# Kernel optimization log

Measured on AMD Instinct MI355X. Metric: run time of the kernel, lower is better.

Reference implementation:

```python
import jax, jax.numpy as jnp
import numpy as np

C = 256   # in_channels
H = 48
W = 48
B = 2     # batch after chunking into 3 frames; input batch = 3*B
F = 3     # frames (torch.chunk(x, 3))
G = 4     # GroupNorm groups
EPS = 1e-6


def setup_inputs() -> dict:
    key = jax.random.key(0)
    ks = jax.random.split(key, 10)
    s = C ** -0.5  # keep q/k magnitudes sane so softmax is not saturated
    return {
        "x":    jax.random.normal(ks[0], (F * B, C, H, W), jnp.float32),
        "gn_w": jnp.ones((C,), jnp.float32),
        "gn_b": jnp.zeros((C,), jnp.float32),
        "wq":   jax.random.normal(ks[1], (C, C), jnp.float32) * s,
        "bq":   jax.random.normal(ks[2], (C,), jnp.float32) * 0.02,
        "wk":   jax.random.normal(ks[3], (C, C), jnp.float32) * s,
        "bk":   jax.random.normal(ks[4], (C,), jnp.float32) * 0.02,
        "wv":   jax.random.normal(ks[5], (C, C), jnp.float32) * s,
        "bv":   jax.random.normal(ks[6], (C,), jnp.float32) * 0.02,
        "wp":   jax.random.normal(ks[7], (C, C), jnp.float32) * s,
        "bp":   jax.random.normal(ks[8], (C,), jnp.float32) * 0.02,
    }


def reference(x, gn_w, gn_b, wq, bq, wk, bk, wv, bv, wp, bp):
    B3, c, h, w = x.shape
    b = B3 // F
    # torch.chunk(x, 3) + stack(dim=2) -> (b, c, f, h, w); chunk index is frame
    hx = jnp.moveaxis(x.reshape(F, b, c, h, w), 0, 2)  # (b, c, f, h, w)

    # GroupNorm(num_groups=4, eps=1e-6, affine)
    hg = hx.reshape(b, G, c // G, F, h, w)
    mu = hg.mean(axis=(2, 3, 4, 5), keepdims=True)
    var = hg.var(axis=(2, 3, 4, 5), keepdims=True)
    hn = ((hg - mu) * jax.lax.rsqrt(var + EPS)).reshape(b, c, F, h, w)
    hn = hn * gn_w[None, :, None, None, None] + gn_b[None, :, None, None, None]

    # 1x1x1 Conv3d == channel matmul over flattened tokens n = (f h w)
    n = F * h * w
    hf = hn.reshape(b, c, n)                                  # (b, c, n)
    q = jnp.einsum('oc,bcn->bon', wq, hf) + bq[None, :, None]
    k = jnp.einsum('oc,bcn->bon', wk, hf) + bk[None, :, None]
    v = jnp.einsum('oc,bcn->bon', wv, hf) + bv[None, :, None]

    # scores[b,n,m] = sum_c q[b,c,n] * k[b,c,m], scaled by c^-0.5, softmax over m
    scores = jnp.einsum('bcn,bcm->bnm', q, k) * (c ** -0.5)
    attn = jax.nn.softmax(scores, axis=-1)                    # (b, n, n)

    # out[b,c,n] = sum_m v[b,c,m] * attn[b,n,m]
    o = jnp.einsum('bcm,bnm->bcn', v, attn)
    o = jnp.einsum('oc,bcn->bon', wp, o) + bp[None, :, None]  # proj_out

    o = o.reshape(b, c, F, h, w)
    # permute(0,2,1,3,4) then merge (b f) -> batch (b-major, f-minor)
    o = jnp.moveaxis(o, 2, 1).reshape(B3, c, h, w)
    return x + o
```

## Files before the change

### kernel.cpp

```cpp
#include <hip/hip_runtime.h>
#include <stdint.h>

#define CDIM 256
#define HW 2304
#define FR 3
#define NBATCH 2
#define NTOK 6912
#define EPSV 1e-6f
#define QSCALE (0.0625f * 1.44269504088896f)

typedef __attribute__((ext_vector_type(8))) short short8;
typedef __attribute__((ext_vector_type(4))) short short4v;
typedef __attribute__((ext_vector_type(4))) float f32x4;
typedef unsigned short u16;

__device__ inline u16 f2bf(float f) {
  union { float f; uint32_t u; } v; v.f = f;
  uint32_t r = v.u + 0x7FFFu + ((v.u >> 16) & 1u);
  return (u16)(r >> 16);
}
__device__ inline float bf2f(u16 h) {
  union { uint32_t u; float f; } v; v.u = ((uint32_t)h) << 16; return v.f;
}
__device__ inline void gload16(const void* g, void* l) {
  __builtin_amdgcn_global_load_lds(
      (const __attribute__((address_space(1))) void*)g,
      (__attribute__((address_space(3))) void*)l, 16, 0, 0);
}

__global__ void pre_k(const float* x, float* part, const float* wq,
                      const float* wk, const float* wv, const float* wp,
                      u16* wb) {
  if (blockIdx.x >= 256) {
    int idx = (blockIdx.x - 256) * 256 + threadIdx.x;
    wb[0 * 65536 + idx] = f2bf(wq[idx] * QSCALE);
    wb[1 * 65536 + idx] = f2bf(wk[idx]);
    wb[2 * 65536 + idx] = f2bf(wv[idx]);
    wb[3 * 65536 + idx] = f2bf(wp[idx]);
    return;
  }
  int bg = blockIdx.x >> 5, sl = blockIdx.x & 31;
  int b = bg >> 2, g = bg & 3;
  int tid = threadIdx.x;
  float s1 = 0.f, s2 = 0.f;
  for (int i = tid; i < 2 * NTOK; i += 256) {
    int cl = sl * 2 + (i / NTOK); int rem = i % NTOK;
    int f = rem / HW; int hw = rem - f * HW;
    float v = x[((size_t)(f * NBATCH + b) * CDIM + g * 64 + cl) * HW + hw];
    s1 += v; s2 += v * v;
  }
  #pragma unroll
  for (int m = 32; m >= 1; m >>= 1) {
    s1 += __shfl_xor(s1, m, 64);
    s2 += __shfl_xor(s2, m, 64);
  }
  __shared__ float r1[4], r2[4];
  int wid = tid >> 6;
  if ((tid & 63) == 0) { r1[wid] = s1; r2[wid] = s2; }
  __syncthreads();
  if (tid == 0) {
    part[blockIdx.x * 2 + 0] = r1[0] + r1[1] + r1[2] + r1[3];
    part[blockIdx.x * 2 + 1] = r2[0] + r2[1] + r2[2] + r2[3];
  }
}

__global__ void gn_fin_k(const float* part, float* stats) {
  int tid = threadIdx.x;
  if (tid < 8) {
    float s1 = 0.f, s2 = 0.f;
    for (int s = 0; s < 32; ++s) {
      s1 += part[(tid * 32 + s) * 2 + 0];
      s2 += part[(tid * 32 + s) * 2 + 1];
    }
    float inv = 1.f / (64.f * NTOK);
    float mu = s1 * inv;
    float var = s2 * inv - mu * mu;
    stats[tid * 2 + 0] = mu;
    stats[tid * 2 + 1] = rsqrtf(var + EPSV);
  }
}

__global__ void gn_apply_k(const float* x, const float* gn_w, const float* gn_b,
                           const float* stats, u16* hn) {
  int nt = blockIdx.x, ct = blockIdx.y, b = blockIdx.z;
  int tid = threadIdx.x;
  __shared__ float tile[64][65];
  int n0 = nt * 64; int f = n0 / HW; int hw0 = n0 - f * HW;
  float mu = stats[(b * 4 + ct) * 2 + 0];
  float rs = stats[(b * 4 + ct) * 2 + 1];
  #pragma unroll
  for (int i = 0; i < 16; ++i) {
    int lin = i * 256 + tid;
    int cr = lin >> 6, nc = lin & 63;
    int c = ct * 64 + cr;
    float v = x[((size_t)(f * NBATCH + b) * CDIM + c) * HW + hw0 + nc];
    tile[cr][nc] = (v - mu) * rs * gn_w[c] + gn_b[c];
  }
  __syncthreads();
  #pragma unroll
  for (int i = 0; i < 16; ++i) {
    int lin = i * 256 + tid;
    int nr = lin >> 6, cc = lin & 63;
    hn[((size_t)b * NTOK + n0 + nr) * CDIM + ct * 64 + cc] = f2bf(tile[cc][nr]);
  }
}

__global__ __launch_bounds__(256) void qkv_k(const u16* hn, const u16* wb,
    const float* bq, const float* bk, const float* bv,
    u16* qb, u16* kb, u16* vb) {
  int nt = blockIdx.x;
  int op = blockIdx.y >> 1, b = blockIdx.y & 1;
  int tid = threadIdx.x, lane = tid & 63, wid = tid >> 6;
  int lr = lane & 15, lg = lane >> 4;
  __shared__ __align__(16) char hn_lds[32768];
  {
    const char* src = (const char*)(hn + ((size_t)b * NTOK + nt * 64) * CDIM);
    #pragma unroll
    for (int i = 0; i < 8; ++i) {
      int off = i * 4096 + wid * 1024 + lane * 16;
      int row = off >> 9;
      gload16(src + (off ^ ((row & 7) << 4)), hn_lds + i * 4096 + wid * 1024);
    }
  }
  __syncthreads();
  f32x4 acc[16];
  #pragma unroll
  for (int i = 0; i < 16; ++i) acc[i] = (f32x4){0.f, 0.f, 0.f, 0.f};
  const u16* wsrc = wb + op * 65536;
  __builtin_amdgcn_s_setprio(1);
  #pragma unroll
  for (int cc = 0; cc < 4; ++cc) {
    short8 afr[2];
    #pragma unroll
    for (int kc = 0; kc < 2; ++kc) {
      int row = wid * 16 + lr;
      int byte = row * 512 + (cc * 64 + kc * 32 + lg * 8) * 2;
      afr[kc] = *(const short8*)(hn_lds + (byte ^ ((row & 7) << 4)));
    }
    #pragma unroll
    for (int cot = 0; cot < 16; ++cot) {
      #pragma unroll
      for (int kc = 0; kc < 2; ++kc) {
        short8 bfr = *(const short8*)(wsrc + (size_t)(cot * 16 + lr) * CDIM +
                                      cc * 64 + kc * 32 + lg * 8);
        if (op == 2)
          acc[cot] = __builtin_amdgcn_mfma_f32_16x16x32_bf16(afr[kc], bfr, acc[cot], 0, 0, 0);
        else
          acc[cot] = __builtin_amdgcn_mfma_f32_16x16x32_bf16(bfr, afr[kc], acc[cot], 0, 0, 0);
      }
    }
  }
  __builtin_amdgcn_s_setprio(0);
  if (op == 2) {
    int m0 = wid * 16 + lg * 4;
    char* vtile = (char*)vb + (size_t)b * NTOK * CDIM * 2 + (size_t)nt * 32768;
    int mchunk = (m0 >> 3);
    #pragma unroll
    for (int cot = 0; cot < 16; ++cot) {
      int co = cot * 16 + lr;
      float bb = bv[co];
      short4v r;
      #pragma unroll
      for (int j = 0; j < 4; ++j) r[j] = (short)f2bf(acc[cot][j] + bb);
      *(short4v*)(vtile + mchunk * 4096 + co * 16 + (lg & 1) * 8) = r;
    }
  } else {
    int row = wid * 16 + lr;
    int n = nt * 64 + row;
    const float* bias = (op == 0) ? bq : bk;
    float bscale = (op == 0) ? QSCALE : 1.0f;
    char* ktile = (char*)kb + (size_t)b * NTOK * CDIM * 2 + (size_t)nt * 32768;
    #pragma unroll
    for (int cot = 0; cot < 16; ++cot) {
      int co = cot * 16 + lg * 4;
      f32x4 b4 = *(const f32x4*)(bias + co);
      short4v r;
      #pragma unroll
      for (int j = 0; j < 4; ++j) r[j] = (short)f2bf(acc[cot][j] + b4[j] * bscale);
      if (op == 0) {
        *(short4v*)(qb + ((size_t)b * NTOK + n) * CDIM + co) = r;
      } else {
        int colchunk = cot * 2 + (lg >> 1);
        *(short4v*)(ktile + colchunk * 1024 + row * 16 + (lg & 1) * 8) = r;
      }
    }
  }
}

template <bool SPLIT>
__global__ __launch_bounds__(768, 3) void flash_k(const u16* qb, const u16* kb,
                                                  const u16* vb, u16* opart,
                                                  float* ml, u16* ob) {
  int qt = blockIdx.x, b = blockIdx.y, sp = blockIdx.z;
  int tid = threadIdx.x, lane = tid & 63, wid = tid >> 6;
  int lr = lane & 15, lg = lane >> 4;
  __shared__ __align__(16) char k_lds[2][32768];
  __shared__ __align__(16) char v_lds[2][32768];
  __shared__ __align__(16) char p_lds[12][2048];

  int t0 = SPLIT ? 36 * sp : 0;
  int t1 = SPLIT ? 36 * sp + 36 : 108;

  short8 aq[8];
  int nq = qt * 192 + wid * 16 + lr;
  const u16* qsrc = qb + ((size_t)b * NTOK + nq) * CDIM;
  #pragma unroll
  for (int kc = 0; kc < 8; ++kc) aq[kc] = *(const short8*)(qsrc + kc * 32 + lg * 8);

  float mrun = -1e30f, lrun = 0.f;
  f32x4 acc[16];
  #pragma unroll
  for (int i = 0; i < 16; ++i) acc[i] = (f32x4){0.f, 0.f, 0.f, 0.f};

  const char* kbb = (const char*)(kb + (size_t)b * NTOK * CDIM);
  const char* vbb = (const char*)(vb + (size_t)b * NTOK * CDIM);
  char* pw = p_lds[wid];
  int kqoff = lg * 1024 + lr * 16;
  int pvoff = lg * 4096 + lr * 16;

  {
    const char* ks = kbb + (size_t)t0 * 32768;
    const char* vs = vbb + (size_t)t0 * 32768;
    for (int ch = wid; ch < 64; ch += 12) {
      if (ch < 32) gload16(ks + ch * 1024 + lane * 16, k_lds[0] + ch * 1024);
      else gload16(vs + (ch - 32) * 1024 + lane * 16, v_lds[0] + (ch - 32) * 1024);
    }
  }
  __syncthreads();

  for (int t = t0; t < t1; ++t) {
    int cur = (t - t0) & 1;
    if (t + 1 < t1) {
      const char* ks = kbb + (size_t)(t + 1) * 32768;
      const char* vs = vbb + (size_t)(t + 1) * 32768;
      for (int ch = wid; ch < 64; ch += 12) {
        if (ch < 32) gload16(ks + ch * 1024 + lane * 16, k_lds[cur ^ 1] + ch * 1024);
        else gload16(vs + (ch - 32) * 1024 + lane * 16, v_lds[cur ^ 1] + (ch - 32) * 1024);
      }
    }
    const char* kcur = k_lds[cur] + kqoff;
    const char* vcur = v_lds[cur] + pvoff;
    f32x4 s[4];
    __builtin_amdgcn_s_setprio(1);
    #pragma unroll
    for (int mt = 0; mt < 4; ++mt) {
      f32x4 a = (f32x4){0.f, 0.f, 0.f, 0.f};
      #pragma unroll
      for (int kc = 0; kc < 8; ++kc) {
        short8 kf = *(const short8*)(kcur + kc * 4096 + mt * 256);
        a = __builtin_amdgcn_mfma_f32_16x16x32_bf16(kf, aq[kc], a, 0, 0, 0);
      }
      s[mt] = a;
    }
    __builtin_amdgcn_s_setprio(0);
    float m0 = fmaxf(fmaxf(s[0][0], s[0][1]), fmaxf(s[0][2], s[0][3]));
    float m1 = fmaxf(fmaxf(s[1][0], s[1][1]), fmaxf(s[1][2], s[1][3]));
    float m2 = fmaxf(fmaxf(s[2][0], s[2][1]), fmaxf(s[2][2], s[2][3]));
    float m3 = fmaxf(fmaxf(s[3][0], s[3][1]), fmaxf(s[3][2], s[3][3]));
    float pmax = fmaxf(fmaxf(m0, m1), fmaxf(m2, m3));
    pmax = fmaxf(pmax, __shfl_xor(pmax, 16, 64));
    pmax = fmaxf(pmax, __shfl_xor(pmax, 32, 64));
    if (__any(pmax > mrun + 6.0f)) {
      float mn = fmaxf(mrun, pmax);
      float r = exp2f(mrun - mn);
      mrun = mn; lrun *= r;
      #pragma unroll
      for (int i = 0; i < 16; ++i) {
        acc[i][0] *= r; acc[i][1] *= r; acc[i][2] *= r; acc[i][3] *= r;
      }
    }
    float ls = 0.f;
    #pragma unroll
    for (int mt = 0; mt < 4; ++mt) {
      #pragma unroll
      for (int j = 0; j < 4; ++j) {
        float p = exp2f(s[mt][j] - mrun);
        s[mt][j] = p;
        ls += p;
      }
    }
    ls += __shfl_xor(ls, 16, 64);
    ls += __shfl_xor(ls, 32, 64);
    lrun += ls;
    #pragma unroll
    for (int mt = 0; mt < 4; ++mt) {
      #pragma unroll
      for (int tp = 0; tp < 2; ++tp) {
        uint32_t pk;
        asm("v_cvt_pk_bf16_f32 %0, %1, %2"
            : "=v"(pk) : "v"(s[mt][2 * tp]), "v"(s[mt][2 * tp + 1]));
        int byte = lr * 128 + mt * 32 + lg * 8 + tp * 4;
        *(uint32_t*)(pw + (byte ^ ((lr & 7) << 4))) = pk;
      }
    }
    __builtin_amdgcn_s_setprio(1);
    #pragma unroll
    for (int mc = 0; mc < 2; ++mc) {
      int pb = lr * 128 + mc * 64 + lg * 16;
      short8 bfr = *(const short8*)(pw + (pb ^ ((lr & 7) << 4)));
      #pragma unroll
      for (int ct = 0; ct < 16; ++ct) {
        short8 av = *(const short8*)(vcur + mc * 16384 + ct * 256);
        acc[ct] = __builtin_amdgcn_mfma_f32_16x16x32_bf16(av, bfr, acc[ct], 0, 0, 0);
      }
    }
    __builtin_amdgcn_s_setprio(0);
    __syncthreads();
  }

  if (!SPLIT) {
    float linv = 1.0f / lrun;
    u16* d0 = ob + ((size_t)b * NTOK + nq) * CDIM;
    #pragma unroll
    for (int ct = 0; ct < 16; ++ct) {
      short4v r;
      #pragma unroll
      for (int j = 0; j < 4; ++j) r[j] = (short)f2bf(acc[ct][j] * linv);
      *(short4v*)(d0 + ct * 16 + lg * 4) = r;
    }
  } else {
    u16* d0 = opart + ((size_t)(sp * 2 + b) * NTOK + nq) * CDIM;
    #pragma unroll
    for (int ct = 0; ct < 16; ++ct) {
      short4v r;
      #pragma unroll
      for (int j = 0; j < 4; ++j) r[j] = (short)f2bf(acc[ct][j]);
      *(short4v*)(d0 + ct * 16 + lg * 4) = r;
    }
    if (lg == 0) {
      size_t mb = (size_t)(sp * 2 + b) * 2;
      ml[(mb + 0) * NTOK + nq] = mrun;
      ml[(mb + 1) * NTOK + nq] = lrun;
    }
  }
}

template <bool SPLIT>
__global__ __launch_bounds__(256) void proj_k(const u16* ob, const u16* opart,
    const float* ml, const u16* wb, const float* bp, const float* x, float* out) {
  int nt = blockIdx.x, b = blockIdx.y;
  int tid = threadIdx.x, lane = tid & 63, wid = tid >> 6;
  int lr = lane & 15, lg = lane >> 4;
  __shared__ __align__(16) char o_lds[32768];
  const u16* wpb = wb + 3 * 65536;
  if (SPLIT) {
    #pragma unroll
    for (int i = 0; i < 8; ++i) {
      int off = i * 4096 + tid * 16;
      int row = off >> 9;
      int c0 = (off & 511) >> 1;
      int n = nt * 64 + row;
      float mm[3], llv[3];
      #pragma unroll
      for (int s = 0; s < 3; ++s) {
        mm[s] = ml[((size_t)(s * 2 + b) * 2 + 0) * NTOK + n];
        llv[s] = ml[((size_t)(s * 2 + b) * 2 + 1) * NTOK + n];
      }
      float M = fmaxf(fmaxf(mm[0], mm[1]), mm[2]);
      float w[3]; float den = 0.f;
      #pragma unroll
      for (int s = 0; s < 3; ++s) { w[s] = exp2f(mm[s] - M); den += w[s] * llv[s]; }
      float inv = 1.f / den;
      float o[8] = {0.f, 0.f, 0.f, 0.f, 0.f, 0.f, 0.f, 0.f};
      #pragma unroll
      for (int s = 0; s < 3; ++s) {
        short8 v = *(const short8*)(opart + ((size_t)(s * 2 + b) * NTOK + n) * CDIM + c0);
        #pragma unroll
        for (int j = 0; j < 8; ++j) o[j] += w[s] * bf2f((u16)v[j]);
      }
      short8 r8;
      #pragma unroll
      for (int j = 0; j < 8; ++j) r8[j] = (short)f2bf(o[j] * inv);
      *(short8*)(o_lds + (off ^ ((row & 7) << 4))) = r8;
    }
  } else {
    const char* src = (const char*)(ob + ((size_t)b * NTOK + nt * 64) * CDIM);
    #pragma unroll
    for (int i = 0; i < 8; ++i) {
      int off = i * 4096 + wid * 1024 + lane * 16;
      int row = off >> 9;
      gload16(src + (off ^ ((row & 7) << 4)), o_lds + i * 4096 + wid * 1024);
    }
  }
  __syncthreads();
  #pragma unroll
  for (int ct2 = 0; ct2 < 4; ++ct2) {
    int cot = wid * 4 + ct2;
    short8 aw[8];
    #pragma unroll
    for (int kc = 0; kc < 8; ++kc)
      aw[kc] = *(const short8*)(wpb + (size_t)(cot * 16 + lr) * CDIM + kc * 32 + lg * 8);
    #pragma unroll
    for (int ntile = 0; ntile < 4; ++ntile) {
      f32x4 a = (f32x4){0.f, 0.f, 0.f, 0.f};
      #pragma unroll
      for (int kc = 0; kc < 8; ++kc) {
        int row = ntile * 16 + lr;
        int byte = row * 512 + (kc * 32 + lg * 8) * 2;
        short8 bfr = *(const short8*)(o_lds + (byte ^ ((row & 7) << 4)));
        a = __builtin_amdgcn_mfma_f32_16x16x32_bf16(aw[kc], bfr, a, 0, 0, 0);
      }
      int n = nt * 64 + ntile * 16 + lr;
      int f = n / HW; int hw = n - f * HW;
      #pragma unroll
      for (int j = 0; j < 4; ++j) {
        int co = cot * 16 + lg * 4 + j;
        float val = a[j] + bp[co];
        size_t oi = ((size_t)(b * FR + f) * CDIM + co) * HW + hw;
        out[oi] = x[oi] + val;
      }
    }
  }
}

extern "C" void kernel_launch(void* const* d_in, const int* in_sizes, int n_in,
                              void* d_out, int out_size, void* d_ws, size_t ws_size,
                              hipStream_t stream) {
  const float* x    = (const float*)d_in[0];
  const float* gn_w = (const float*)d_in[1];
  const float* gn_b = (const float*)d_in[2];
  const float* wq   = (const float*)d_in[3];
  const float* bq   = (const float*)d_in[4];
  const float* wk   = (const float*)d_in[5];
  const float* bk   = (const float*)d_in[6];
  const float* wv   = (const float*)d_in[7];
  const float* bv   = (const float*)d_in[8];
  const float* wp   = (const float*)d_in[9];
  const float* bp   = (const float*)d_in[10];
  float* out = (float*)d_out;
  char* ws = (char*)d_ws;

  float* stats = (float*)(ws + 0);
  float* part  = (float*)(ws + 256);
  u16* wb = (u16*)(ws + 4096);
  u16* hn = (u16*)(ws + 528384);
  u16* qb = (u16*)(ws + 7606272);
  u16* kb = (u16*)(ws + 14684160);
  u16* vb = (u16*)(ws + 21762048);
  u16* ob = (u16*)(ws + 28839936);
  u16* opart = (u16*)(ws + 35917824);
  float* ml  = (float*)(ws + 57151488);
  const size_t NEED_SPLIT = 57483264;

  pre_k<<<512, 256, 0, stream>>>(x, part, wq, wk, wv, wp, wb);
  gn_fin_k<<<1, 64, 0, stream>>>(part, stats);
  gn_apply_k<<<dim3(108, 4, 2), 256, 0, stream>>>(x, gn_w, gn_b, stats, hn);
  qkv_k<<<dim3(108, 6), 256, 0, stream>>>(hn, wb, bq, bk, bv, qb, kb, vb);
  if (ws_size >= NEED_SPLIT) {
    flash_k<true><<<dim3(36, 2, 3), 768, 0, stream>>>(qb, kb, vb, opart, ml, ob);
    proj_k<true><<<dim3(108, 2), 256, 0, stream>>>(ob, opart, ml, wb, bp, x, out);
  } else {
    flash_k<false><<<dim3(36, 2, 1), 768, 0, stream>>>(qb, kb, vb, opart, ml, ob);
    proj_k<false><<<dim3(108, 2), 256, 0, stream>>>(ob, opart, ml, wb, bp, x, out);
  }
}
```

Before: 227.2 us.

## Rewrite flash attention with 32x32x16 MFMA and in-register P via permlane swap

Result: faster. 216.3 us, median of 2 (-4.8%).

```diff
diff --git a/kernel.cpp b/kernel.cpp
--- a/kernel.cpp
+++ b/kernel.cpp
@@ -12,6 +12,8 @@
 typedef __attribute__((ext_vector_type(8))) short short8;
 typedef __attribute__((ext_vector_type(4))) short short4v;
 typedef __attribute__((ext_vector_type(4))) float f32x4;
+typedef __attribute__((ext_vector_type(16))) float f32x16;
+typedef __attribute__((ext_vector_type(4))) uint32_t u32x4;
 typedef unsigned short u16;
 
 __device__ inline u16 f2bf(float f) {
@@ -188,42 +190,45 @@
 }
 
 template <bool SPLIT>
-__global__ __launch_bounds__(768, 3) void flash_k(const u16* qb, const u16* kb,
+__global__ __launch_bounds__(512, 2) void flash_k(const u16* qb, const u16* kb,
                                                   const u16* vb, u16* opart,
                                                   float* ml, u16* ob) {
   int qt = blockIdx.x, b = blockIdx.y, sp = blockIdx.z;
   int tid = threadIdx.x, lane = tid & 63, wid = tid >> 6;
-  int lr = lane & 15, lg = lane >> 4;
+  int ln = lane & 31, hi = lane >> 5;
   __shared__ __align__(16) char k_lds[2][32768];
   __shared__ __align__(16) char v_lds[2][32768];
-  __shared__ __align__(16) char p_lds[12][2048];
-
-  int t0 = SPLIT ? 36 * sp : 0;
-  int t1 = SPLIT ? 36 * sp + 36 : 108;
-
-  short8 aq[8];
-  int nq = qt * 192 + wid * 16 + lr;
+
+  int t0 = SPLIT ? 27 * sp : 0;
+  int t1 = SPLIT ? 27 * sp + 27 : 108;
+
+  int nq = qt * 256 + wid * 32 + ln;
   const u16* qsrc = qb + ((size_t)b * NTOK + nq) * CDIM;
-  #pragma unroll
-  for (int kc = 0; kc < 8; ++kc) aq[kc] = *(const short8*)(qsrc + kc * 32 + lg * 8);
+  short8 qf[16];
+  #pragma unroll
+  for (int ks = 0; ks < 16; ++ks)
+    qf[ks] = *(const short8*)(qsrc + ks * 16 + hi * 8);
 
   float mrun = -1e30f, lrun = 0.f;
-  f32x4 acc[16];
-  #pragma unroll
-  for (int i = 0; i < 16; ++i) acc[i] = (f32x4){0.f, 0.f, 0.f, 0.f};
+  f32x16 o[8];
+  #pragma unroll
+  for (int i = 0; i < 8; ++i)
+    #pragma unroll
+    for (int j = 0; j < 16; ++j) o[i][j] = 0.f;
 
   const char* kbb = (const char*)(kb + (size_t)b * NTOK * CDIM);
   const char* vbb = (const char*)(vb + (size_t)b * NTOK * CDIM);
-  char* pw = p_lds[wid];
-  int kqoff = lg * 1024 + lr * 16;
-  int pvoff = lg * 4096 + lr * 16;
+  int kbase = hi * 1024 + ln * 16;
+  int vbase = hi * 4096 + ln * 16;
 
   {
-    const char* ks = kbb + (size_t)t0 * 32768;
-    const char* vs = vbb + (size_t)t0 * 32768;
-    for (int ch = wid; ch < 64; ch += 12) {
-      if (ch < 32) gload16(ks + ch * 1024 + lane * 16, k_lds[0] + ch * 1024);
-      else gload16(vs + (ch - 32) * 1024 + lane * 16, v_lds[0] + (ch - 32) * 1024);
+    const char* ks_ = kbb + (size_t)t0 * 32768;
+    const char* vs_ = vbb + (size_t)t0 * 32768;
+    #pragma unroll
+    for (int i = 0; i < 8; ++i) {
+      int ch = i * 8 + wid;
+      if (ch < 32) gload16(ks_ + ch * 1024 + lane * 16, k_lds[0] + ch * 1024);
+      else gload16(vs_ + (ch - 32) * 1024 + lane * 16, v_lds[0] + (ch - 32) * 1024);
     }
   }
   __syncthreads();
@@ -231,80 +236,72 @@
   for (int t = t0; t < t1; ++t) {
     int cur = (t - t0) & 1;
     if (t + 1 < t1) {
-      const char* ks = kbb + (size_t)(t + 1) * 32768;
-      const char* vs = vbb + (size_t)(t + 1) * 32768;
-      for (int ch = wid; ch < 64; ch += 12) {
-        if (ch < 32) gload16(ks + ch * 1024 + lane * 16, k_lds[cur ^ 1] + ch * 1024);
-        else gload16(vs + (ch - 32) * 1024 + lane * 16, v_lds[cur ^ 1] + (ch - 32) * 1024);
-      }
-    }
-    const char* kcur = k_lds[cur] + kqoff;
-    const char* vcur = v_lds[cur] + pvoff;
-    f32x4 s[4];
-    __builtin_amdgcn_s_setprio(1);
-    #pragma unroll
-    for (int mt = 0; mt < 4; ++mt) {
-      f32x4 a = (f32x4){0.f, 0.f, 0.f, 0.f};
-      #pragma unroll
-      for (int kc = 0; kc < 8; ++kc) {
-        short8 kf = *(const short8*)(kcur + kc * 4096 + mt * 256);
-        a = __builtin_amdgcn_mfma_f32_16x16x32_bf16(kf, aq[kc], a, 0, 0, 0);
-      }
-      s[mt] = a;
-    }
-    __builtin_amdgcn_s_setprio(0);
-    float m0 = fmaxf(fmaxf(s[0][0], s[0][1]), fmaxf(s[0][2], s[0][3]));
-    float m1 = fmaxf(fmaxf(s[1][0], s[1][1]), fmaxf(s[1][2], s[1][3]));
-    float m2 = fmaxf(fmaxf(s[2][0], s[2][1]), fmaxf(s[2][2], s[2][3]));
-    float m3 = fmaxf(fmaxf(s[3][0], s[3][1]), fmaxf(s[3][2], s[3][3]));
-    float pmax = fmaxf(fmaxf(m0, m1), fmaxf(m2, m3));
-    pmax = fmaxf(pmax, __shfl_xor(pmax, 16, 64));
-    pmax = fmaxf(pmax, __shfl_xor(pmax, 32, 64));
-    if (__any(pmax > mrun + 6.0f)) {
-      float mn = fmaxf(mrun, pmax);
-      float r = exp2f(mrun - mn);
-      mrun = mn; lrun *= r;
-      #pragma unroll
-      for (int i = 0; i < 16; ++i) {
-        acc[i][0] *= r; acc[i][1] *= r; acc[i][2] *= r; acc[i][3] *= r;
-      }
-    }
-    float ls = 0.f;
-    #pragma unroll
-    for (int mt = 0; mt < 4; ++mt) {
-      #pragma unroll
-      for (int j = 0; j < 4; ++j) {
-        float p = exp2f(s[mt][j] - mrun);
-        s[mt][j] = p;
-        ls += p;
-      }
-    }
-    ls += __shfl_xor(ls, 16, 64);
-    ls += __shfl_xor(ls, 32, 64);
-    lrun += ls;
-    #pragma unroll
-    for (int mt = 0; mt < 4; ++mt) {
-      #pragma unroll
-      for (int tp = 0; tp < 2; ++tp) {
-        uint32_t pk;
-        asm("v_cvt_pk_bf16_f32 %0, %1, %2"
-            : "=v"(pk) : "v"(s[mt][2 * tp]), "v"(s[mt][2 * tp + 1]));
-        int byte = lr * 128 + mt * 32 + lg * 8 + tp * 4;
-        *(uint32_t*)(pw + (byte ^ ((lr & 7) << 4))) = pk;
-      }
-    }
-    __builtin_amdgcn_s_setprio(1);
-    #pragma unroll
-    for (int mc = 0; mc < 2; ++mc) {
-      int pb = lr * 128 + mc * 64 + lg * 16;
-      short8 bfr = *(const short8*)(pw + (pb ^ ((lr & 7) << 4)));
-      #pragma unroll
-      for (int ct = 0; ct < 16; ++ct) {
-        short8 av = *(const short8*)(vcur + mc * 16384 + ct * 256);
-        acc[ct] = __builtin_amdgcn_mfma_f32_16x16x32_bf16(av, bfr, acc[ct], 0, 0, 0);
-      }
-    }
-    __builtin_amdgcn_s_setprio(0);
+      const char* ks_ = kbb + (size_t)(t + 1) * 32768;
+      const char* vs_ = vbb + (size_t)(t + 1) * 32768;
+      #pragma unroll
+      for (int i = 0; i < 8; ++i) {
+        int ch = i * 8 + wid;
+        if (ch < 32) gload16(ks_ + ch * 1024 + lane * 16, k_lds[cur ^ 1] + ch * 1024);
+        else gload16(vs_ + (ch - 32) * 1024 + lane * 16, v_lds[cur ^ 1] + (ch - 32) * 1024);
+      }
+    }
+    const char* kc = k_lds[cur] + kbase;
+    const char* vc = v_lds[cur] + vbase;
+
+    #pragma unroll
+    for (int mt = 0; mt < 2; ++mt) {
+      f32x16 S;
+      #pragma unroll
+      for (int j = 0; j < 16; ++j) S[j] = 0.f;
+      __builtin_amdgcn_s_setprio(1);
+      #pragma unroll
+      for (int ks = 0; ks < 16; ++ks) {
+        short8 kf = *(const short8*)(kc + ks * 2048 + mt * 512);
+        S = __builtin_amdgcn_mfma_f32_32x32x16_bf16(kf, qf[ks], S, 0, 0, 0);
+      }
+      __builtin_amdgcn_s_setprio(0);
+      float px = S[0];
+      #pragma unroll
+      for (int j = 1; j < 16; ++j) px = fmaxf(px, S[j]);
+      px = fmaxf(px, __shfl_xor(px, 32, 64));
+      if (__any(px > mrun + 10.0f)) {
+        float mn = fmaxf(mrun, px);
+        float r = exp2f(mrun - mn);
+        mrun = mn; lrun *= r;
+        #pragma unroll
+        for (int i = 0; i < 8; ++i)
+          #pragma unroll
+          for (int j = 0; j < 16; ++j) o[i][j] *= r;
+      }
+      float lsum = 0.f;
+      #pragma unroll
+      for (int j = 0; j < 16; ++j) {
+        float p = exp2f(S[j] - mrun);
+        S[j] = p; lsum += p;
+      }
+      lsum += __shfl_xor(lsum, 32, 64);
+      lrun += lsum;
+      #pragma unroll
+      for (int lks = 0; lks < 2; ++lks) {
+        int rb = lks * 8;
+        uint32_t x0, x1, y0, y1;
+        asm("v_cvt_pk_bf16_f32 %0, %1, %2" : "=v"(x0) : "v"(S[rb + 0]), "v"(S[rb + 1]));
+        asm("v_cvt_pk_bf16_f32 %0, %1, %2" : "=v"(x1) : "v"(S[rb + 2]), "v"(S[rb + 3]));
+        asm("v_cvt_pk_bf16_f32 %0, %1, %2" : "=v"(y0) : "v"(S[rb + 4]), "v"(S[rb + 5]));
+        asm("v_cvt_pk_bf16_f32 %0, %1, %2" : "=v"(y1) : "v"(S[rb + 6]), "v"(S[rb + 7]));
+        asm("v_permlane32_swap_b32 %0, %1" : "+v"(x0), "+v"(y0));
+        asm("v_permlane32_swap_b32 %0, %1" : "+v"(x1), "+v"(y1));
+        u32x4 pd = (u32x4){x0, x1, y0, y1};
+        short8 pf = *(short8*)&pd;
+        __builtin_amdgcn_s_setprio(1);
+        #pragma unroll
+        for (int ct = 0; ct < 8; ++ct) {
+          short8 vf = *(const short8*)(vc + (mt * 2 + lks) * 8192 + ct * 512);
+          o[ct] = __builtin_amdgcn_mfma_f32_32x32x16_bf16(vf, pf, o[ct], 0, 0, 0);
+        }
+        __builtin_amdgcn_s_setprio(0);
+      }
+    }
     __syncthreads();
   }
 
@@ -312,22 +309,28 @@
     float linv = 1.0f / lrun;
     u16* d0 = ob + ((size_t)b * NTOK + nq) * CDIM;
     #pragma unroll
-    for (int ct = 0; ct < 16; ++ct) {
-      short4v r;
-      #pragma unroll
-      for (int j = 0; j < 4; ++j) r[j] = (short)f2bf(acc[ct][j] * linv);
-      *(short4v*)(d0 + ct * 16 + lg * 4) = r;
+    for (int ct = 0; ct < 8; ++ct) {
+      #pragma unroll
+      for (int rq = 0; rq < 4; ++rq) {
+        short4v r4;
+        #pragma unroll
+        for (int j = 0; j < 4; ++j) r4[j] = (short)f2bf(o[ct][rq * 4 + j] * linv);
+        *(short4v*)(d0 + ct * 32 + rq * 8 + hi * 4) = r4;
+      }
     }
   } else {
     u16* d0 = opart + ((size_t)(sp * 2 + b) * NTOK + nq) * CDIM;
     #pragma unroll
-    for (int ct = 0; ct < 16; ++ct) {
-      short4v r;
-      #pragma unroll
-      for (int j = 0; j < 4; ++j) r[j] = (short)f2bf(acc[ct][j]);
-      *(short4v*)(d0 + ct * 16 + lg * 4) = r;
-    }
-    if (lg == 0) {
+    for (int ct = 0; ct < 8; ++ct) {
+      #pragma unroll
+      for (int rq = 0; rq < 4; ++rq) {
+        short4v r4;
+        #pragma unroll
+        for (int j = 0; j < 4; ++j) r4[j] = (short)f2bf(o[ct][rq * 4 + j]);
+        *(short4v*)(d0 + ct * 32 + rq * 8 + hi * 4) = r4;
+      }
+    }
+    if (hi == 0) {
       size_t mb = (size_t)(sp * 2 + b) * 2;
       ml[(mb + 0) * NTOK + nq] = mrun;
       ml[(mb + 1) * NTOK + nq] = lrun;
@@ -350,20 +353,20 @@
       int row = off >> 9;
       int c0 = (off & 511) >> 1;
       int n = nt * 64 + row;
-      float mm[3], llv[3];
-      #pragma unroll
-      for (int s = 0; s < 3; ++s) {
+      float mm[4], llv[4];
+      #pragma unroll
+      for (int s = 0; s < 4; ++s) {
         mm[s] = ml[((size_t)(s * 2 + b) * 2 + 0) * NTOK + n];
         llv[s] = ml[((size_t)(s * 2 + b) * 2 + 1) * NTOK + n];
       }
-      float M = fmaxf(fmaxf(mm[0], mm[1]), mm[2]);
-      float w[3]; float den = 0.f;
-      #pragma unroll
-      for (int s = 0; s < 3; ++s) { w[s] = exp2f(mm[s] - M); den += w[s] * llv[s]; }
+      float M = fmaxf(fmaxf(mm[0], mm[1]), fmaxf(mm[2], mm[3]));
+      float w[4]; float den = 0.f;
+      #pragma unroll
+      for (int s = 0; s < 4; ++s) { w[s] = exp2f(mm[s] - M); den += w[s] * llv[s]; }
       float inv = 1.f / den;
       float o[8] = {0.f, 0.f, 0.f, 0.f, 0.f, 0.f, 0.f, 0.f};
       #pragma unroll
-      for (int s = 0; s < 3; ++s) {
+      for (int s = 0; s < 4; ++s) {
         short8 v = *(const short8*)(opart + ((size_t)(s * 2 + b) * NTOK + n) * CDIM + c0);
         #pragma unroll
         for (int j = 0; j < 8; ++j) o[j] += w[s] * bf2f((u16)v[j]);
@@ -439,18 +442,18 @@
   u16* vb = (u16*)(ws + 21762048);
   u16* ob = (u16*)(ws + 28839936);
   u16* opart = (u16*)(ws + 35917824);
-  float* ml  = (float*)(ws + 57151488);
-  const size_t NEED_SPLIT = 57483264;
+  float* ml  = (float*)(ws + 64229376);
+  const size_t NEED_SPLIT = 64671744;
 
   pre_k<<<512, 256, 0, stream>>>(x, part, wq, wk, wv, wp, wb);
   gn_fin_k<<<1, 64, 0, stream>>>(part, stats);
   gn_apply_k<<<dim3(108, 4, 2), 256, 0, stream>>>(x, gn_w, gn_b, stats, hn);
   qkv_k<<<dim3(108, 6), 256, 0, stream>>>(hn, wb, bq, bk, bv, qb, kb, vb);
   if (ws_size >= NEED_SPLIT) {
-    flash_k<true><<<dim3(36, 2, 3), 768, 0, stream>>>(qb, kb, vb, opart, ml, ob);
+    flash_k<true><<<dim3(27, 2, 4), 512, 0, stream>>>(qb, kb, vb, opart, ml, ob);
     proj_k<true><<<dim3(108, 2), 256, 0, stream>>>(ob, opart, ml, wb, bp, x, out);
   } else {
-    flash_k<false><<<dim3(36, 2, 1), 768, 0, stream>>>(qb, kb, vb, opart, ml, ob);
+    flash_k<false><<<dim3(27, 2, 1), 512, 0, stream>>>(qb, kb, vb, opart, ml, ob);
     proj_k<false><<<dim3(108, 2), 256, 0, stream>>>(ob, opart, ml, wb, bp, x, out);
   }
 }
```
